# Kernel optimization log

Hardware: AMD Instinct MI355X
Metric: run time of the kernel (lower is better)

Reference implementation:

```python
import jax, jax.numpy as jnp
import numpy as np

B, Q, C, H, N, D, F = 1, 2048, 2048, 1024, 16, 64, 4096
R = Q + C  # relative position encoding length
EPS = 1e-12
NEG = 1e30


def setup_inputs() -> dict:
    key = jax.random.key(0)
    ks = jax.random.split(key, 16)
    s = 0.02
    return dict(
        content_stream=jax.random.normal(ks[0], (B, Q, H), jnp.float32),
        content_mask=jnp.zeros((B, 1, Q, C), jnp.float32),
        context=jax.random.normal(ks[1], (B, C, H), jnp.float32),
        position_encoding=jax.random.normal(ks[2], (B, R, H), jnp.float32),
        content_bias=jax.random.normal(ks[3], (N, D), jnp.float32) * s,
        position_bias=jax.random.normal(ks[4], (N, D), jnp.float32) * s,
        segment_encoding=jax.random.normal(ks[5], (2, N, D), jnp.float32) * s,
        segment_matrix=jax.random.randint(ks[6], (B, Q, C), 0, 2).astype(bool),
        segment_bias=jax.random.normal(ks[7], (N, D), jnp.float32) * s,
        Wq=jax.random.normal(ks[8], (H, N, D), jnp.float32) * s,
        Wk=jax.random.normal(ks[9], (H, N, D), jnp.float32) * s,
        Wv=jax.random.normal(ks[10], (H, N, D), jnp.float32) * s,
        Wr=jax.random.normal(ks[11], (H, N, D), jnp.float32) * s,
        Wo=jax.random.normal(ks[12], (H, N, D), jnp.float32) * s,
        ln1_gamma=jnp.ones((H,), jnp.float32),
        ln1_beta=jnp.zeros((H,), jnp.float32),
        W1=jax.random.normal(ks[13], (H, F), jnp.float32) * s,
        b1=jnp.zeros((F,), jnp.float32),
        W2=jax.random.normal(ks[14], (F, H), jnp.float32) * s,
        b2=jnp.zeros((H,), jnp.float32),
        ln2_gamma=jnp.ones((H,), jnp.float32),
        ln2_beta=jnp.zeros((H,), jnp.float32),
    )


def _layernorm(x, g, b):
    m = jnp.mean(x, axis=-1, keepdims=True)
    v = jnp.mean(jnp.square(x - m), axis=-1, keepdims=True)
    return (x - m) * jax.lax.rsqrt(v + EPS) * g + b


def _rel_shift(x, klen):
    # x: [b, n, q, r] -> shifted [b, n, q, klen] (XLNet reshape trick)
    b, n, q, r = x.shape
    x = x.reshape(b, n, r, q)[:, :, 1:, :].reshape(b, n, q, r - 1)
    return x[:, :, :, :klen]


def reference(content_stream, content_mask, context, position_encoding,
              content_bias, position_bias, segment_encoding, segment_matrix,
              segment_bias, Wq, Wk, Wv, Wr, Wo, ln1_gamma, ln1_beta,
              W1, b1, W2, b2, ln2_gamma, ln2_beta):
    q = jnp.einsum('bqh,hnd->bqnd', content_stream, Wq)
    k = jnp.einsum('bch,hnd->bcnd', context, Wk)
    v = jnp.einsum('bch,hnd->bcnd', context, Wv)
    r = jnp.einsum('brh,hnd->brnd', position_encoding, Wr)

    # content / position / segment bias terms (XLNet relative attention)
    ac = jnp.einsum('bqnd,bcnd->bnqc', q + content_bias, k)
    bd = _rel_shift(jnp.einsum('bqnd,brnd->bnqr', q + position_bias, r),
                    k.shape[1])
    ef = jnp.einsum('bqnd,snd->bnqs', q + segment_bias, segment_encoding)
    ef = jnp.where(segment_matrix[:, None], ef[..., 1:], ef[..., :1])

    scores = (ac + bd + ef) / jnp.sqrt(jnp.float32(D))
    scores = scores - NEG * content_mask  # mask: 1.0 = disallowed
    probs = jax.nn.softmax(scores, axis=-1)

    attn = jnp.einsum('bnqc,bcnd->bqnd', probs, v)
    attn_out = jnp.einsum('bqnd,hnd->bqh', attn, Wo)

    # residual + LN, then FFN, residual + LN (dropout off: training=False)
    ffn_in = _layernorm(attn_out + content_stream, ln1_gamma, ln1_beta)
    ffn_out = jax.nn.relu(ffn_in @ W1 + b1) @ W2 + b2
    return _layernorm(ffn_out + ffn_in, ln2_gamma, ln2_beta)
```

## Files before the change

kernel.cpp:

```cpp
#include <hip/hip_runtime.h>
#include <stdint.h>


typedef unsigned short ushort_t;
typedef __attribute__((ext_vector_type(8))) short bf16x8;
typedef __attribute__((ext_vector_type(4))) float f32x4;

#define QLEN 2048
#define CLEN 2048
#define HDIM 1024
#define NHEAD 16
#define DHEAD 64
#define RLEN 4096
#define FDIM 4096

__device__ __forceinline__ float bf2f(ushort_t u) {
  union { float f; uint32_t i; } x; x.i = ((uint32_t)u) << 16; return x.f;
}
__device__ __forceinline__ ushort_t f2bf(float f) {
  union { float f; uint32_t i; } x; x.f = f;
  uint32_t r = x.i + 0x7fffu + ((x.i >> 16) & 1u);
  return (ushort_t)(r >> 16);
}
__device__ __forceinline__ f32x4 mfma16(bf16x8 a, bf16x8 b, f32x4 c) {
  return __builtin_amdgcn_mfma_f32_16x16x32_bf16(a, b, c, 0, 0, 0);
}
__device__ __forceinline__ bool probe_bf16(const uint32_t* probe) {
  return probe[0] == 0x3F803F80u;
}

typedef const __attribute__((address_space(1))) void* gas_t;
typedef __attribute__((address_space(3))) void* las_t;
__device__ __forceinline__ void glds16(const void* g, void* l) {
  __builtin_amdgcn_global_load_lds((gas_t)(uintptr_t)g, (las_t)(uintptr_t)l, 16, 0, 0);
}

__device__ __forceinline__ void bar_lds() {
  __asm__ volatile("s_waitcnt lgkmcnt(0)\n\ts_barrier" ::: "memory");
}
__device__ __forceinline__ void bar_full() {
  __asm__ volatile("s_waitcnt vmcnt(0) lgkmcnt(0)\n\ts_barrier" ::: "memory");
}

struct ConvJobs {
  const void* src[5];
  const void* mask_src;
  ushort_t* dst[5];
  int n[5];
  int blk0[6];
};

__global__ __launch_bounds__(256) void conv_all(
    ConvJobs J, const uint32_t* __restrict__ probe)
{
  const bool isb = probe_bf16(probe);
  int j = 0;
  #pragma unroll
  for (int t = 1; t < 5; t++) if ((int)blockIdx.x >= J.blk0[t]) j = t;
  const int lb = blockIdx.x - J.blk0[j];
  const int nb = J.blk0[j + 1] - J.blk0[j];
  const int n = J.n[j];
  ushort_t* dst = J.dst[j];
  if (j < 4) {
    const void* src = J.src[j];
    for (int i = lb * 256 + threadIdx.x; i < n; i += nb * 256)
      dst[i] = isb ? ((const ushort_t*)src)[i] : f2bf(((const float*)src)[i]);
  } else {
    const void* sm = J.src[4];
    uint32_t sw = 0;
    #pragma unroll
    for (int t = 0; t < 8; t++) sw |= ((const uint32_t*)sm)[t];
    const bool i8 = sw > 1u;
    for (int i = lb * 256 + threadIdx.x; i < n; i += nb * 256) {
      const int s = i8 ? (int)((const unsigned char*)sm)[i]
                       : (int)((const uint32_t*)sm)[i];
      const float mv = isb ? bf2f(((const ushort_t*)J.mask_src)[i])
                           : ((const float*)J.mask_src)[i];
      const float f = (float)(s ? 1 : 0) + (mv != 0.f ? 2.f : 0.f);
      dst[i] = f2bf(f);
    }
  }
}

struct SmallBatch {
  const void* src[10];
  int n[10];
  int off[10];
};

__global__ __launch_bounds__(256) void convert_small(
    SmallBatch sb, ushort_t* __restrict__ dst, const uint32_t* __restrict__ probe)
{
  const bool isb = probe_bf16(probe);
  const int t = blockIdx.x;
  const void* s = sb.src[t];
  ushort_t* d = dst + sb.off[t];
  for (int i = threadIdx.x; i < sb.n[t]; i += 256)
    d[i] = isb ? ((const ushort_t*)s)[i] : f2bf(((const float*)s)[i]);
}

struct TransJobs { const void* src[4]; ushort_t* dst[4]; };
__global__ __launch_bounds__(256) void transpose4_to_bf16(
    TransJobs T, int R, int C, const uint32_t* __restrict__ probe)
{
  const bool isb = probe_bf16(probe);
  const void* in = T.src[blockIdx.z];
  ushort_t* out = T.dst[blockIdx.z];
  __shared__ ushort_t t[32][33];
  const int bx = blockIdx.x * 32, by = blockIdx.y * 32;
  const int x = threadIdx.x & 31, y0 = threadIdx.x >> 5;
  #pragma unroll
  for (int yy = 0; yy < 32; yy += 8) {
    const size_t idx = (size_t)(by + y0 + yy) * C + bx + x;
    t[y0 + yy][x] = isb ? ((const ushort_t*)in)[idx] : f2bf(((const float*)in)[idx]);
  }
  __syncthreads();
  #pragma unroll
  for (int yy = 0; yy < 32; yy += 8)
    out[(size_t)(bx + y0 + yy) * R + by + x] = t[x][y0 + yy];
}

__global__ __launch_bounds__(256) void transpose_to_bf16(
    const void* __restrict__ in, ushort_t* __restrict__ out, int R, int C,
    const uint32_t* __restrict__ probe)
{
  const bool isb = probe_bf16(probe);
  __shared__ ushort_t t[32][33];
  const int bx = blockIdx.x * 32, by = blockIdx.y * 32;
  const int x = threadIdx.x & 31, y0 = threadIdx.x >> 5;
  #pragma unroll
  for (int yy = 0; yy < 32; yy += 8) {
    const size_t idx = (size_t)(by + y0 + yy) * C + bx + x;
    t[y0 + yy][x] = isb ? ((const ushort_t*)in)[idx] : f2bf(((const float*)in)[idx]);
  }
  __syncthreads();
  #pragma unroll
  for (int yy = 0; yy < 32; yy += 8)
    out[(size_t)(bx + y0 + yy) * R + by + x] = t[x][y0 + yy];
}

__device__ __forceinline__ void gemm_store(
    void* out, const ushort_t* bias, int M, int N, int epi,
    int gm, int gn, float v)
{
  if (epi == 0) {
    ((ushort_t*)out)[(size_t)gm * N + gn] = f2bf(v);
  } else if (epi == 1) {
    ((ushort_t*)out)[(size_t)gn * M + gm] = f2bf(v);
  } else if (epi == 2) {
    ((float*)out)[(size_t)gm * N + gn] = v;
  } else if (epi == 3) {
    v += bf2f(bias[gn]); v = v > 0.f ? v : 0.f;
    ((ushort_t*)out)[(size_t)gm * N + gn] = f2bf(v);
  } else if (epi == 4) {
    v += bf2f(bias[gn]);
    ((float*)out)[(size_t)gm * N + gn] = v;
  } else if (epi == 5) {
    ((ushort_t*)out)[((size_t)(gn >> 6) * M + gm) * 64 + (gn & 63)] = f2bf(v);
  } else {
    if (gn < 1024)
      ((ushort_t*)out)[((size_t)(gn >> 6) * M + gm) * 64 + (gn & 63)] = f2bf(v);
    else
      ((ushort_t*)out)[(size_t)2097152 + (size_t)(gn - 1024) * M + gm] = f2bf(v);
  }
}

__global__ __launch_bounds__(256) void gemm_bt_kernel(
    const ushort_t* __restrict__ A, const ushort_t* __restrict__ Bt,
    const ushort_t* __restrict__ bias, void* __restrict__ out,
    int M, int N, int K, int epi)
{
  __shared__ __attribute__((aligned(16))) ushort_t As[2][128 * 32];
  __shared__ __attribute__((aligned(16))) ushort_t Bs[2][64 * 32];
  const int tid = threadIdx.x;
  const int lane = tid & 63, wave = tid >> 6;
  const int l15 = lane & 15, quad = lane >> 4;
  const int m0 = blockIdx.y * 128, n0 = blockIdx.x * 64;

  const int arow = tid >> 2;
  const int acol = (tid & 3) * 8;

  f32x4 acc[2][4];
  #pragma unroll
  for (int i = 0; i < 2; i++)
    #pragma unroll
    for (int j = 0; j < 4; j++) acc[i][j] = (f32x4){0.f, 0.f, 0.f, 0.f};

  const int KI = K >> 5;
  glds16(&A[(size_t)(m0 + arow) * K + acol], &As[0][tid * 8]);
  glds16(&A[(size_t)(m0 + arow + 64) * K + acol], &As[0][tid * 8 + 2048]);
  glds16(&Bt[(size_t)(n0 + arow) * K + acol], &Bs[0][tid * 8]);
  bar_full();

  for (int ki = 0; ki < KI; ki++) {
    const int b = ki & 1;
    if (ki + 1 < KI) {
      const int k1 = (ki + 1) << 5;
      glds16(&A[(size_t)(m0 + arow) * K + k1 + acol], &As[b ^ 1][tid * 8]);
      glds16(&A[(size_t)(m0 + arow + 64) * K + k1 + acol], &As[b ^ 1][tid * 8 + 2048]);
      glds16(&Bt[(size_t)(n0 + arow) * K + k1 + acol], &Bs[b ^ 1][tid * 8]);
    }
    bf16x8 af[2], bfr[4];
    #pragma unroll
    for (int i = 0; i < 2; i++)
      af[i] = *(const bf16x8*)&As[b][(wave * 32 + i * 16 + l15) * 32 + quad * 8];
    #pragma unroll
    for (int j = 0; j < 4; j++)
      bfr[j] = *(const bf16x8*)&Bs[b][(j * 16 + l15) * 32 + quad * 8];
    #pragma unroll
    for (int i = 0; i < 2; i++)
      #pragma unroll
      for (int j = 0; j < 4; j++)
        acc[i][j] = mfma16(af[i], bfr[j], acc[i][j]);
    bar_full();
  }

  #pragma unroll
  for (int i = 0; i < 2; i++)
    #pragma unroll
    for (int j = 0; j < 4; j++)
      #pragma unroll
      for (int rg = 0; rg < 4; rg++)
        gemm_store(out, bias, M, N, epi,
                   m0 + wave * 32 + i * 16 + quad * 4 + rg,
                   n0 + j * 16 + l15, acc[i][j][rg]);
}

struct Ptr4 { void* p[4]; };
__global__ __launch_bounds__(256) void gemm128_bt_kernel(
    const ushort_t* __restrict__ A, const ushort_t* __restrict__ Bt,
    const ushort_t* __restrict__ bias, Ptr4 outs,
    int M, int N, int K, int Kc, int epi)
{
  __shared__ __attribute__((aligned(16))) ushort_t As[2][128 * 32];
  __shared__ __attribute__((aligned(16))) ushort_t Bs[2][128 * 32];
  const int tid = threadIdx.x;
  const int lane = tid & 63, wave = tid >> 6;
  const int l15 = lane & 15, quad = lane >> 4;
  const int wm = wave >> 1, wn = wave & 1;
  const int m0 = blockIdx.y * 128, n0 = blockIdx.x * 128;
  const int kb = blockIdx.z * Kc;
  void* out = outs.p[blockIdx.z];

  const int arow = tid >> 2;
  const int acol = (tid & 3) * 8;

  f32x4 acc[4][4];
  #pragma unroll
  for (int i = 0; i < 4; i++)
    #pragma unroll
    for (int j = 0; j < 4; j++) acc[i][j] = (f32x4){0.f, 0.f, 0.f, 0.f};

  const int KI = Kc >> 5;
  glds16(&A[(size_t)(m0 + arow) * K + kb + acol], &As[0][tid * 8]);
  glds16(&A[(size_t)(m0 + arow + 64) * K + kb + acol], &As[0][tid * 8 + 2048]);
  glds16(&Bt[(size_t)(n0 + arow) * K + kb + acol], &Bs[0][tid * 8]);
  glds16(&Bt[(size_t)(n0 + arow + 64) * K + kb + acol], &Bs[0][tid * 8 + 2048]);
  bar_full();

  for (int ki = 0; ki < KI; ki++) {
    const int b = ki & 1;
    if (ki + 1 < KI) {
      const int k1 = kb + ((ki + 1) << 5);
      glds16(&A[(size_t)(m0 + arow) * K + k1 + acol], &As[b ^ 1][tid * 8]);
      glds16(&A[(size_t)(m0 + arow + 64) * K + k1 + acol], &As[b ^ 1][tid * 8 + 2048]);
      glds16(&Bt[(size_t)(n0 + arow) * K + k1 + acol], &Bs[b ^ 1][tid * 8]);
      glds16(&Bt[(size_t)(n0 + arow + 64) * K + k1 + acol], &Bs[b ^ 1][tid * 8 + 2048]);
    }
    bf16x8 af[4], bfr[4];
    #pragma unroll
    for (int i = 0; i < 4; i++)
      af[i] = *(const bf16x8*)&As[b][(wm * 64 + i * 16 + l15) * 32 + quad * 8];
    #pragma unroll
    for (int j = 0; j < 4; j++)
      bfr[j] = *(const bf16x8*)&Bs[b][(wn * 64 + j * 16 + l15) * 32 + quad * 8];
    #pragma unroll
    for (int i = 0; i < 4; i++)
      #pragma unroll
      for (int j = 0; j < 4; j++)
        acc[i][j] = mfma16(af[i], bfr[j], acc[i][j]);
    bar_full();
  }

  #pragma unroll
  for (int i = 0; i < 4; i++)
    #pragma unroll
    for (int j = 0; j < 4; j++)
      #pragma unroll
      for (int rg = 0; rg < 4; rg++)
        gemm_store(out, bias, M, N, epi,
                   m0 + wm * 64 + i * 16 + quad * 4 + rg,
                   n0 + wn * 64 + j * 16 + l15, acc[i][j][rg]);
}

__global__ __launch_bounds__(256) void gemm64_bt_kernel(
    const ushort_t* __restrict__ A, const ushort_t* __restrict__ Bt,
    const ushort_t* __restrict__ bias, void* __restrict__ out,
    int M, int N, int K, int epi)
{
  __shared__ __attribute__((aligned(16))) ushort_t As[2][64 * 32];
  __shared__ __attribute__((aligned(16))) ushort_t Bs[2][64 * 32];
  const int tid = threadIdx.x;
  const int lane = tid & 63, wave = tid >> 6;
  const int l15 = lane & 15, quad = lane >> 4;
  const int wm = wave >> 1, wn = wave & 1;
  const int m0 = blockIdx.y * 64, n0 = blockIdx.x * 64;

  const int arow = tid >> 2;
  const int acol = (tid & 3) * 8;

  f32x4 acc[2][2];
  #pragma unroll
  for (int i = 0; i < 2; i++)
    #pragma unroll
    for (int j = 0; j < 2; j++) acc[i][j] = (f32x4){0.f, 0.f, 0.f, 0.f};

  const int KI = K >> 5;
  glds16(&A[(size_t)(m0 + arow) * K + acol], &As[0][tid * 8]);
  glds16(&Bt[(size_t)(n0 + arow) * K + acol], &Bs[0][tid * 8]);
  bar_full();

  for (int ki = 0; ki < KI; ki++) {
    const int b = ki & 1;
    if (ki + 1 < KI) {
      const int k1 = (ki + 1) << 5;
      glds16(&A[(size_t)(m0 + arow) * K + k1 + acol], &As[b ^ 1][tid * 8]);
      glds16(&Bt[(size_t)(n0 + arow) * K + k1 + acol], &Bs[b ^ 1][tid * 8]);
    }
    bf16x8 af[2], bfr[2];
    #pragma unroll
    for (int i = 0; i < 2; i++)
      af[i] = *(const bf16x8*)&As[b][(wm * 32 + i * 16 + l15) * 32 + quad * 8];
    #pragma unroll
    for (int j = 0; j < 2; j++)
      bfr[j] = *(const bf16x8*)&Bs[b][(wn * 32 + j * 16 + l15) * 32 + quad * 8];
    #pragma unroll
    for (int i = 0; i < 2; i++)
      #pragma unroll
      for (int j = 0; j < 2; j++)
        acc[i][j] = mfma16(af[i], bfr[j], acc[i][j]);
    bar_full();
  }

  #pragma unroll
  for (int i = 0; i < 2; i++)
    #pragma unroll
    for (int j = 0; j < 2; j++)
      #pragma unroll
      for (int rg = 0; rg < 4; rg++)
        gemm_store(out, bias, M, N, epi,
                   m0 + wm * 32 + i * 16 + quad * 4 + rg,
                   n0 + wn * 32 + j * 16 + l15, acc[i][j][rg]);
}

#define ESTR 36
#define PSTR2 72
__global__ __launch_bounds__(256, 2) void attn_flash(
    const ushort_t* __restrict__ qh, const ushort_t* __restrict__ kh,
    const ushort_t* __restrict__ vT, const ushort_t* __restrict__ rh,
    const ushort_t* __restrict__ cbias, const ushort_t* __restrict__ pbias,
    const ushort_t* __restrict__ sbias, const ushort_t* __restrict__ senc,
    const ushort_t* __restrict__ fmb, ushort_t* __restrict__ attn)
{
  __shared__ __attribute__((aligned(16))) ushort_t kbuf[2][64 * 64];
  __shared__ __attribute__((aligned(16))) ushort_t vbuf[2][64 * 64];
  __shared__ __attribute__((aligned(16))) ushort_t rbuf[2][96 * 64];
  __shared__ __attribute__((aligned(16))) ushort_t Pbuf[32 * PSTR2];
  __shared__ __attribute__((aligned(16))) float escr[4 * 16 * ESTR];
  __shared__ float wsum[4][32];
  __shared__ float e0s[32], e1s[32];

  const int n = blockIdx.x;
  const int q0 = blockIdx.y * 32;
  const int tid = threadIdx.x;
  const int lane = tid & 63, wave = tid >> 6;
  const int l15 = lane & 15, quad = lane >> 4;

  const ushort_t* qn = qh + (size_t)n * QLEN * 64;
  const ushort_t* kn = kh + (size_t)n * CLEN * 64;
  const ushort_t* rn = rh + (size_t)n * RLEN * 64;
  const ushort_t* vn = vT + (size_t)n * 64 * CLEN;

  const int srow = lane >> 3;
  const int sg = (lane & 7) ^ srow;

  ushort_t* qpcS = (ushort_t*)escr;
  ushort_t* qppS = qpcS + 32 * 64;
  for (int idx = tid; idx < 32 * 64; idx += 256) {
    const int row = idx >> 6, col = idx & 63;
    const float qv = bf2f(qn[(size_t)(q0 + row) * 64 + col]);
    qpcS[idx] = f2bf(qv + bf2f(cbias[n * DHEAD + col]));
    qppS[idx] = f2bf(qv + bf2f(pbias[n * DHEAD + col]));
  }
  if (wave == 3) {
    const int row = lane & 31, sidx = lane >> 5;
    float a = 0.f;
    for (int d = 0; d < DHEAD; d++)
      a += (bf2f(qn[(size_t)(q0 + row) * 64 + d]) + bf2f(sbias[n * DHEAD + d]))
           * bf2f(senc[(size_t)(sidx * NHEAD + n) * DHEAD + d]);
    if (sidx == 0) e0s[row] = a; else e1s[row] = a;
  }
  __syncthreads();

  const bf16x8* qpc8 = (const bf16x8*)qpcS;
  const bf16x8* qpp8 = (const bf16x8*)qppS;
  bf16x8 qcf[2][2], qpf[2][2];
  #pragma unroll
  for (int hq = 0; hq < 2; hq++)
    #pragma unroll
    for (int h = 0; h < 2; h++) {
      qcf[hq][h] = qpc8[(hq * 16 + l15) * 8 + h * 4 + quad];
      qpf[hq][h] = qpp8[(hq * 16 + l15) * 8 + h * 4 + quad];
    }

  {
    const int c0 = 0, ua = c0 - q0 + (QLEN - 32);
    if (wave == 0) {
      #pragma unroll
      for (int i = 0; i < 8; i++)
        glds16(kn + (size_t)(c0 + i * 8 + srow) * 64 + sg * 8, &kbuf[0][i * 512]);
    } else if (wave == 1) {
      #pragma unroll
      for (int i = 0; i < 8; i++)
        glds16(vn + (size_t)(i * 8 + srow) * CLEN + c0 + sg * 8, &vbuf[0][i * 512]);
    } else if (wave == 2) {
      #pragma unroll
      for (int i = 0; i < 8; i++)
        glds16(rn + (size_t)(ua + i * 8 + srow) * 64 + sg * 8, &rbuf[0][i * 512]);
    } else {
      #pragma unroll
      for (int i = 0; i < 4; i++)
        glds16(rn + (size_t)(ua + 64 + i * 8 + srow) * 64 + sg * 8, &rbuf[0][(64 + i * 8) * 64]);
    }
  }
  bar_full();

  float a0q[2], adq[2];
  #pragma unroll
  for (int hq = 0; hq < 2; hq++) {
    const float e0 = e0s[hq * 16 + l15], e1 = e1s[hq * 16 + l15];
    a0q[hq] = e0 * 0.125f;
    adq[hq] = (e1 - e0) * 0.125f;
  }

  float* escr_w = escr + wave * (16 * ESTR);
  const int gk0 = quad ^ (l15 & 7);
  const int gk1 = (quad + 4) ^ (l15 & 7);

  float l_row[2] = {0.f, 0.f};
  f32x4 O[2];
  O[0] = (f32x4){0.f, 0.f, 0.f, 0.f};
  O[1] = (f32x4){0.f, 0.f, 0.f, 0.f};

  const size_t eo0 = (size_t)(q0 + l15) * CLEN + wave * 16 + quad * 4;
  const size_t eo1 = eo0 + (size_t)16 * CLEN;

  for (int ci = 0; ci < CLEN / 64; ci++) {
    const int b = ci & 1;

    uint2 fmv[2];
    fmv[0] = *(const uint2*)&fmb[eo0 + (size_t)ci * 64];
    fmv[1] = *(const uint2*)&fmb[eo1 + (size_t)ci * 64];

    if (ci + 1 < CLEN / 64) {
      const int c1 = (ci + 1) * 64, ua1 = c1 - q0 + (QLEN - 32);
      if (wave == 0) {
        #pragma unroll
        for (int i = 0; i < 8; i++)
          glds16(kn + (size_t)(c1 + i * 8 + srow) * 64 + sg * 8, &kbuf[b ^ 1][i * 512]);
      } else if (wave == 1) {
        #pragma unroll
        for (int i = 0; i < 8; i++)
          glds16(vn + (size_t)(i * 8 + srow) * CLEN + c1 + sg * 8, &vbuf[b ^ 1][i * 512]);
      } else if (wave == 2) {
        #pragma unroll
        for (int i = 0; i < 8; i++)
          glds16(rn + (size_t)(ua1 + i * 8 + srow) * 64 + sg * 8, &rbuf[b ^ 1][i * 512]);
      } else {
        #pragma unroll
        for (int i = 0; i < 4; i++)
          glds16(rn + (size_t)(ua1 + 64 + i * 8 + srow) * 64 + sg * 8, &rbuf[b ^ 1][(64 + i * 8) * 64]);
      }
    }

    const int krow = wave * 16 + l15;
    const bf16x8 kf0 = *(const bf16x8*)&kbuf[b][krow * 64 + gk0 * 8];
    const bf16x8 kf1 = *(const bf16x8*)&kbuf[b][krow * 64 + gk1 * 8];

    #pragma unroll
    for (int hq = 0; hq < 2; hq++) {
      #pragma unroll
      for (int t = 0; t < 2; t++) {
        const int rrow = wave * 16 + ((1 - hq) + t) * 16 + l15;
        f32x4 e = (f32x4){0.f, 0.f, 0.f, 0.f};
        e = mfma16(*(const bf16x8*)&rbuf[b][rrow * 64 + gk0 * 8], qpf[hq][0], e);
        e = mfma16(*(const bf16x8*)&rbuf[b][rrow * 64 + gk1 * 8], qpf[hq][1], e);
        *(f32x4*)&escr_w[l15 * ESTR + t * 16 + quad * 4] = e;
      }

      f32x4 a = (f32x4){0.f, 0.f, 0.f, 0.f};
      a = mfma16(kf0, qcf[hq][0], a);
      a = mfma16(kf1, qcf[hq][1], a);

      const uint2 fv = fmv[hq];
      const ushort_t fm4[4] = {(ushort_t)(fv.x & 0xffff), (ushort_t)(fv.x >> 16),
                               (ushort_t)(fv.y & 0xffff), (ushort_t)(fv.y >> 16)};
      const float* dg = &escr_w[l15 * ESTR + quad * 4 - l15 + 16];
      float p[4], psum = 0.f;
      #pragma unroll
      for (int rg = 0; rg < 4; rg++) {
        const float f = bf2f(fm4[rg]);
        const float mk = floorf(f * 0.5f);
        const float sm = f - 2.f * mk;
        float v = fmaf(a[rg] + dg[rg], 0.125f, fmaf(sm, adq[hq], a0q[hq]));
        v = fmaf(mk, -1.0e30f, v);
        p[rg] = __expf(v);
        psum += p[rg];
      }
      psum += __shfl_xor(psum, 16);
      psum += __shfl_xor(psum, 32);
      l_row[hq] += psum;

      uint2 pk;
      pk.x = (uint32_t)f2bf(p[0]) | ((uint32_t)f2bf(p[1]) << 16);
      pk.y = (uint32_t)f2bf(p[2]) | ((uint32_t)f2bf(p[3]) << 16);
      *(uint2*)&Pbuf[(hq * 16 + l15) * PSTR2 + wave * 16 + quad * 4] = pk;
    }
    bar_lds();

    const int vrow = wave * 16 + l15;
    const bf16x8 vf0 = *(const bf16x8*)&vbuf[b][vrow * 64 + gk0 * 8];
    const bf16x8 vf1 = *(const bf16x8*)&vbuf[b][vrow * 64 + gk1 * 8];
    #pragma unroll
    for (int hq = 0; hq < 2; hq++) {
      const bf16x8 pa0 = *(const bf16x8*)&Pbuf[(hq * 16 + l15) * PSTR2 + quad * 8];
      const bf16x8 pa1 = *(const bf16x8*)&Pbuf[(hq * 16 + l15) * PSTR2 + 32 + quad * 8];
      O[hq] = mfma16(pa0, vf0, O[hq]);
      O[hq] = mfma16(pa1, vf1, O[hq]);
    }

    bar_full();
  }

  if (quad == 0) { wsum[wave][l15] = l_row[0]; wsum[wave][16 + l15] = l_row[1]; }
  __syncthreads();
  #pragma unroll
  for (int hq = 0; hq < 2; hq++) {
    const int qi = hq * 16 + l15;
    const float l = wsum[0][qi] + wsum[1][qi] + wsum[2][qi] + wsum[3][qi];
    const float linv = 1.0f / l;
    float linv4[4];
    #pragma unroll
    for (int rg = 0; rg < 4; rg++) linv4[rg] = __shfl(linv, quad * 4 + rg);
    #pragma unroll
    for (int rg = 0; rg < 4; rg++)
      attn[(size_t)(q0 + hq * 16 + quad * 4 + rg) * HDIM + n * 64 + wave * 16 + l15] =
          f2bf(O[hq][rg] * linv4[rg]);
  }
}

__global__ __launch_bounds__(256) void ln_kernel(
    const float* __restrict__ x0, const float* __restrict__ x1,
    const float* __restrict__ x2, const float* __restrict__ x3,
    const ushort_t* __restrict__ res_bf, const float* __restrict__ res_f,
    const ushort_t* __restrict__ badd,
    const ushort_t* __restrict__ gamma, const ushort_t* __restrict__ beta,
    ushort_t* __restrict__ out_bf, float* __restrict__ out_f,
    void* __restrict__ out_dyn, const uint32_t* __restrict__ probe)
{
  const int row = blockIdx.x, tid = threadIdx.x;
  const int lane = tid & 63, wave = tid >> 6;
  __shared__ float red[8];
  const size_t base = (size_t)row * HDIM;
  float v[4];
  #pragma unroll
  for (int i = 0; i < 4; i++) {
    const int h = tid + i * 256;
    float xv = x0[base + h];
    if (x1) xv += x1[base + h] + x2[base + h] + x3[base + h];
    if (badd) xv += bf2f(badd[h]);
    const float rv = res_bf ? bf2f(res_bf[base + h]) : res_f[base + h];
    v[i] = xv + rv;
  }
  float s = v[0] + v[1] + v[2] + v[3];
  float ss = v[0] * v[0] + v[1] * v[1] + v[2] * v[2] + v[3] * v[3];
  #pragma unroll
  for (int off = 32; off > 0; off >>= 1) {
    s += __shfl_xor(s, off);
    ss += __shfl_xor(ss, off);
  }
  if (lane == 0) { red[wave] = s; red[4 + wave] = ss; }
  __syncthreads();
  s = red[0] + red[1] + red[2] + red[3];
  ss = red[4] + red[5] + red[6] + red[7];
  const float mean = s * (1.0f / HDIM);
  float var = ss * (1.0f / HDIM) - mean * mean;
  var = var > 0.f ? var : 0.f;
  const float rs = rsqrtf(var + 1e-12f);
  const bool outb = out_dyn ? probe_bf16(probe) : false;
  #pragma unroll
  for (int i = 0; i < 4; i++) {
    const int h = tid + i * 256;
    const float y = (v[i] - mean) * rs * bf2f(gamma[h]) + bf2f(beta[h]);
    if (out_bf) out_bf[base + h] = f2bf(y);
    if (out_f)  out_f[base + h] = y;
    if (out_dyn) {
      if (outb) ((ushort_t*)out_dyn)[base + h] = f2bf(y);
      else      ((float*)out_dyn)[base + h] = y;
    }
  }
}

extern "C" void kernel_launch(void* const* d_in, const int* in_sizes, int n_in,
                              void* d_out, int out_size, void* d_ws, size_t ws_size,
                              hipStream_t stream)
{
  (void)in_sizes; (void)n_in; (void)out_size; (void)ws_size;

  const void* cs_r   = d_in[0];
  const void* mask_r = d_in[1];
  const void* ctx_r  = d_in[2];
  const void* pe_r   = d_in[3];
  const void* cb_r   = d_in[4];
  const void* pb_r   = d_in[5];
  const void* senc_r = d_in[6];
  const void* smat   = d_in[7];
  const void* sb_r   = d_in[8];
  const void* Wq_r   = d_in[9];
  const void* Wk_r   = d_in[10];
  const void* Wv_r   = d_in[11];
  const void* Wr_r   = d_in[12];
  const void* Wo_r   = d_in[13];
  const void* g1_r   = d_in[14];
  const void* be1_r  = d_in[15];
  const void* W1_r   = d_in[16];
  const void* b1_r   = d_in[17];
  const void* W2_r   = d_in[18];
  const void* b2_r   = d_in[19];
  const void* g2_r   = d_in[20];
  const void* be2_r  = d_in[21];

  const uint32_t* probe = (const uint32_t*)g1_r;

  char* w = (char*)d_ws;
  #define WSOFF(mb) ((void*)(w + ((size_t)(mb) << 20)))
  ushort_t* fm_b     = (ushort_t*)WSOFF(0);
  ushort_t* Wqt      = (ushort_t*)WSOFF(8);
  ushort_t* Wkt      = (ushort_t*)WSOFF(10);
  ushort_t* Wvt      = (ushort_t*)WSOFF(12);
  ushort_t* Wrt      = (ushort_t*)WSOFF(14);
  ushort_t* W1t      = (ushort_t*)WSOFF(16);
  ushort_t* W2t      = (ushort_t*)WSOFF(24);
  ushort_t* Wo_b     = (ushort_t*)WSOFF(32);
  ushort_t* smalls   = (ushort_t*)WSOFF(34);
  ushort_t* cs_b     = (ushort_t*)WSOFF(35);
  ushort_t* ctx_b    = (ushort_t*)WSOFF(47);
  ushort_t* pe_b     = (ushort_t*)WSOFF(51);
  ushort_t* qbuf     = (ushort_t*)WSOFF(59);
  ushort_t* kbuf     = (ushort_t*)WSOFF(63);
  ushort_t* vTbuf    = (ushort_t*)WSOFF(67);
  ushort_t* rbuf     = (ushort_t*)WSOFF(71);
  ushort_t* attnbuf  = (ushort_t*)WSOFF(79);
  float*    attn_out = (float*)WSOFF(83);
  ushort_t* ffn_in_b = (ushort_t*)WSOFF(91);
  ushort_t* hidden   = (ushort_t*)WSOFF(39);
  float*    ffn_in_f = (float*)WSOFF(71);
  float*    fp0      = (float*)WSOFF(0);
  float*    fp1      = (float*)WSOFF(8);
  float*    fp2      = (float*)WSOFF(59);
  float*    fp3      = (float*)WSOFF(83);

  ushort_t* cb   = smalls + 0;
  ushort_t* pb   = smalls + 1024;
  ushort_t* sb   = smalls + 2048;
  ushort_t* senc = smalls + 3072;
  ushort_t* b1   = smalls + 5120;
  ushort_t* b2   = smalls + 9216;
  ushort_t* g1   = smalls + 10240;
  ushort_t* be1  = smalls + 11264;
  ushort_t* g2   = smalls + 12288;
  ushort_t* be2  = smalls + 13312;

  const dim3 blk(256);

  SmallBatch sbatch;
  const void* ssrc[10] = {cb_r, pb_r, sb_r, senc_r, b1_r, b2_r, g1_r, be1_r, g2_r, be2_r};
  const int   sn[10]   = {1024, 1024, 1024, 2048, 4096, 1024, 1024, 1024, 1024, 1024};
  const int   soff[10] = {0, 1024, 2048, 3072, 5120, 9216, 10240, 11264, 12288, 13312};
  for (int i = 0; i < 10; i++) { sbatch.src[i] = ssrc[i]; sbatch.n[i] = sn[i]; sbatch.off[i] = soff[i]; }
  convert_small<<<10, blk, 0, stream>>>(sbatch, smalls, probe);

  ConvJobs cj;
  cj.src[0] = cs_r;  cj.dst[0] = cs_b;  cj.n[0] = QLEN * HDIM;
  cj.src[1] = ctx_r; cj.dst[1] = ctx_b; cj.n[1] = CLEN * HDIM;
  cj.src[2] = pe_r;  cj.dst[2] = pe_b;  cj.n[2] = RLEN * HDIM;
  cj.src[3] = Wo_r;  cj.dst[3] = Wo_b;  cj.n[3] = HDIM * HDIM;
  cj.src[4] = smat;  cj.dst[4] = fm_b;  cj.n[4] = QLEN * CLEN;
  cj.mask_src = mask_r;
  int pfx = 0;
  for (int i = 0; i < 5; i++) {
    cj.blk0[i] = pfx;
    pfx += (cj.n[i] + 2047) / 2048;
  }
  cj.blk0[5] = pfx;
  conv_all<<<pfx, blk, 0, stream>>>(cj, probe);

  TransJobs tj;
  tj.src[0] = Wq_r; tj.dst[0] = Wqt;
  tj.src[1] = Wk_r; tj.dst[1] = Wkt;
  tj.src[2] = Wv_r; tj.dst[2] = Wvt;
  tj.src[3] = Wr_r; tj.dst[3] = Wrt;
  transpose4_to_bf16<<<dim3(32, 32, 4), blk, 0, stream>>>(tj, HDIM, HDIM, probe);
  transpose_to_bf16<<<dim3(128, 32), blk, 0, stream>>>(W1_r, W1t, HDIM, FDIM, probe);
  transpose_to_bf16<<<dim3(32, 128), blk, 0, stream>>>(W2_r, W2t, FDIM, HDIM, probe);

  gemm64_bt_kernel<<<dim3(16, 32), blk, 0, stream>>>(cs_b,  Wqt, nullptr, qbuf,  QLEN, HDIM, HDIM, 5);
  gemm_bt_kernel<<<dim3(32, 16), blk, 0, stream>>>(ctx_b, Wkt, nullptr, kbuf, CLEN, 2048, HDIM, 6);
  gemm_bt_kernel<<<dim3(16, 32), blk, 0, stream>>>(pe_b,  Wrt, nullptr, rbuf,  RLEN, HDIM, HDIM, 5);

  attn_flash<<<dim3(NHEAD, QLEN / 32), blk, 0, stream>>>(
      qbuf, kbuf, vTbuf, rbuf, cb, pb, sb, senc, fm_b, attnbuf);

  gemm64_bt_kernel<<<dim3(16, 32), blk, 0, stream>>>(attnbuf, Wo_b, nullptr, attn_out, QLEN, HDIM, HDIM, 2);

  ln_kernel<<<QLEN, blk, 0, stream>>>(attn_out, nullptr, nullptr, nullptr,
                                      cs_b, nullptr, nullptr, g1, be1,
                                      ffn_in_b, ffn_in_f, nullptr, probe);

  Ptr4 o1; o1.p[0] = hidden; o1.p[1] = o1.p[2] = o1.p[3] = nullptr;
  gemm128_bt_kernel<<<dim3(32, 16, 1), blk, 0, stream>>>(
      ffn_in_b, W1t, b1, o1, QLEN, FDIM, HDIM, HDIM, 3);

  Ptr4 o2; o2.p[0] = fp0; o2.p[1] = fp1; o2.p[2] = fp2; o2.p[3] = fp3;
  gemm128_bt_kernel<<<dim3(8, 16, 4), blk, 0, stream>>>(
      hidden, W2t, nullptr, o2, QLEN, HDIM, FDIM, FDIM / 4, 2);

  ln_kernel<<<QLEN, blk, 0, stream>>>(fp0, fp1, fp2, fp3,
                                      nullptr, ffn_in_f, b2, g2, be2,
                                      nullptr, nullptr, d_out, probe);
  #undef WSOFF
}
```

Baseline: 489.8 us.

## Split attention query halves across eight waves per block

The attention kernel now launches 512 threads per block instead of 256. The 2x2 query-half loop is spread over eight waves, so each wave handles one 16-row query half and one 16-column key slice, and the K/V/R tile loads are split across all eight waves. This roughly halves the per-wave serial work and register pressure and raises the number of waves that can hide latency. In exchange it adds shared scratch, doubles the waves taking part in each barrier, and issues smaller load chunks per wave.

Result: faster. 475.4 us (-2.9%).

```diff
diff --git a/kernel.cpp b/kernel.cpp
--- a/kernel.cpp
+++ b/kernel.cpp
@@ -355,7 +355,7 @@
 
 #define ESTR 36
 #define PSTR2 72
-__global__ __launch_bounds__(256, 2) void attn_flash(
+__global__ __launch_bounds__(512, 4) void attn_flash(
     const ushort_t* __restrict__ qh, const ushort_t* __restrict__ kh,
     const ushort_t* __restrict__ vT, const ushort_t* __restrict__ rh,
     const ushort_t* __restrict__ cbias, const ushort_t* __restrict__ pbias,
@@ -366,8 +366,8 @@
   __shared__ __attribute__((aligned(16))) ushort_t vbuf[2][64 * 64];
   __shared__ __attribute__((aligned(16))) ushort_t rbuf[2][96 * 64];
   __shared__ __attribute__((aligned(16))) ushort_t Pbuf[32 * PSTR2];
-  __shared__ __attribute__((aligned(16))) float escr[4 * 16 * ESTR];
-  __shared__ float wsum[4][32];
+  __shared__ __attribute__((aligned(16))) float escr[8 * 16 * ESTR];
+  __shared__ float wsum[2][4][16];
   __shared__ float e0s[32], e1s[32];
 
   const int n = blockIdx.x;
@@ -375,6 +375,7 @@
   const int tid = threadIdx.x;
   const int lane = tid & 63, wave = tid >> 6;
   const int l15 = lane & 15, quad = lane >> 4;
+  const int hq = wave >> 2, ct = wave & 3;
 
   const ushort_t* qn = qh + (size_t)n * QLEN * 64;
   const ushort_t* kn = kh + (size_t)n * CLEN * 64;
@@ -386,13 +387,13 @@
 
   ushort_t* qpcS = (ushort_t*)escr;
   ushort_t* qppS = qpcS + 32 * 64;
-  for (int idx = tid; idx < 32 * 64; idx += 256) {
+  for (int idx = tid; idx < 32 * 64; idx += 512) {
     const int row = idx >> 6, col = idx & 63;
     const float qv = bf2f(qn[(size_t)(q0 + row) * 64 + col]);
     qpcS[idx] = f2bf(qv + bf2f(cbias[n * DHEAD + col]));
     qppS[idx] = f2bf(qv + bf2f(pbias[n * DHEAD + col]));
   }
-  if (wave == 3) {
+  if (wave == 7) {
     const int row = lane & 31, sidx = lane >> 5;
     float a = 0.f;
     for (int d = 0; d < DHEAD; d++)
@@ -404,159 +405,134 @@
 
   const bf16x8* qpc8 = (const bf16x8*)qpcS;
   const bf16x8* qpp8 = (const bf16x8*)qppS;
-  bf16x8 qcf[2][2], qpf[2][2];
-  #pragma unroll
-  for (int hq = 0; hq < 2; hq++)
-    #pragma unroll
-    for (int h = 0; h < 2; h++) {
-      qcf[hq][h] = qpc8[(hq * 16 + l15) * 8 + h * 4 + quad];
-      qpf[hq][h] = qpp8[(hq * 16 + l15) * 8 + h * 4 + quad];
-    }
+  bf16x8 qcf[2], qpf[2];
+  #pragma unroll
+  for (int h = 0; h < 2; h++) {
+    qcf[h] = qpc8[(hq * 16 + l15) * 8 + h * 4 + quad];
+    qpf[h] = qpp8[(hq * 16 + l15) * 8 + h * 4 + quad];
+  }
 
   {
     const int c0 = 0, ua = c0 - q0 + (QLEN - 32);
-    if (wave == 0) {
-      #pragma unroll
-      for (int i = 0; i < 8; i++)
-        glds16(kn + (size_t)(c0 + i * 8 + srow) * 64 + sg * 8, &kbuf[0][i * 512]);
-    } else if (wave == 1) {
-      #pragma unroll
-      for (int i = 0; i < 8; i++)
-        glds16(vn + (size_t)(i * 8 + srow) * CLEN + c0 + sg * 8, &vbuf[0][i * 512]);
-    } else if (wave == 2) {
-      #pragma unroll
-      for (int i = 0; i < 8; i++)
-        glds16(rn + (size_t)(ua + i * 8 + srow) * 64 + sg * 8, &rbuf[0][i * 512]);
+    if (wave < 2) {
+      const int r0 = wave * 32;
+      #pragma unroll
+      for (int i = 0; i < 4; i++)
+        glds16(kn + (size_t)(c0 + r0 + i * 8 + srow) * 64 + sg * 8, &kbuf[0][(r0 + i * 8) * 64]);
+    } else if (wave < 4) {
+      const int r0 = (wave - 2) * 32;
+      #pragma unroll
+      for (int i = 0; i < 4; i++)
+        glds16(vn + (size_t)(r0 + i * 8 + srow) * CLEN + c0 + sg * 8, &vbuf[0][(r0 + i * 8) * 64]);
     } else {
-      #pragma unroll
-      for (int i = 0; i < 4; i++)
-        glds16(rn + (size_t)(ua + 64 + i * 8 + srow) * 64 + sg * 8, &rbuf[0][(64 + i * 8) * 64]);
+      const int r0 = (wave - 4) * 24;
+      #pragma unroll
+      for (int i = 0; i < 3; i++)
+        glds16(rn + (size_t)(ua + r0 + i * 8 + srow) * 64 + sg * 8, &rbuf[0][(r0 + i * 8) * 64]);
     }
   }
   bar_full();
 
-  float a0q[2], adq[2];
-  #pragma unroll
-  for (int hq = 0; hq < 2; hq++) {
-    const float e0 = e0s[hq * 16 + l15], e1 = e1s[hq * 16 + l15];
-    a0q[hq] = e0 * 0.125f;
-    adq[hq] = (e1 - e0) * 0.125f;
-  }
+  const float e0v = e0s[hq * 16 + l15], e1v = e1s[hq * 16 + l15];
+  const float a0q = e0v * 0.125f;
+  const float adq = (e1v - e0v) * 0.125f;
 
   float* escr_w = escr + wave * (16 * ESTR);
   const int gk0 = quad ^ (l15 & 7);
   const int gk1 = (quad + 4) ^ (l15 & 7);
 
-  float l_row[2] = {0.f, 0.f};
-  f32x4 O[2];
-  O[0] = (f32x4){0.f, 0.f, 0.f, 0.f};
-  O[1] = (f32x4){0.f, 0.f, 0.f, 0.f};
-
-  const size_t eo0 = (size_t)(q0 + l15) * CLEN + wave * 16 + quad * 4;
-  const size_t eo1 = eo0 + (size_t)16 * CLEN;
+  float l_row = 0.f;
+  f32x4 O = (f32x4){0.f, 0.f, 0.f, 0.f};
+
+  const size_t eoff = (size_t)(q0 + hq * 16 + l15) * CLEN + ct * 16 + quad * 4;
 
   for (int ci = 0; ci < CLEN / 64; ci++) {
     const int b = ci & 1;
 
-    uint2 fmv[2];
-    fmv[0] = *(const uint2*)&fmb[eo0 + (size_t)ci * 64];
-    fmv[1] = *(const uint2*)&fmb[eo1 + (size_t)ci * 64];
+    const uint2 fmv = *(const uint2*)&fmb[eoff + (size_t)ci * 64];
 
     if (ci + 1 < CLEN / 64) {
       const int c1 = (ci + 1) * 64, ua1 = c1 - q0 + (QLEN - 32);
-      if (wave == 0) {
-        #pragma unroll
-        for (int i = 0; i < 8; i++)
-          glds16(kn + (size_t)(c1 + i * 8 + srow) * 64 + sg * 8, &kbuf[b ^ 1][i * 512]);
-      } else if (wave == 1) {
-        #pragma unroll
-        for (int i = 0; i < 8; i++)
-          glds16(vn + (size_t)(i * 8 + srow) * CLEN + c1 + sg * 8, &vbuf[b ^ 1][i * 512]);
-      } else if (wave == 2) {
-        #pragma unroll
-        for (int i = 0; i < 8; i++)
-          glds16(rn + (size_t)(ua1 + i * 8 + srow) * 64 + sg * 8, &rbuf[b ^ 1][i * 512]);
-      } else {
+      if (wave < 2) {
+        const int r0 = wave * 32;
         #pragma unroll
         for (int i = 0; i < 4; i++)
-          glds16(rn + (size_t)(ua1 + 64 + i * 8 + srow) * 64 + sg * 8, &rbuf[b ^ 1][(64 + i * 8) * 64]);
+          glds16(kn + (size_t)(c1 + r0 + i * 8 + srow) * 64 + sg * 8, &kbuf[b ^ 1][(r0 + i * 8) * 64]);
+      } else if (wave < 4) {
+        const int r0 = (wave - 2) * 32;
+        #pragma unroll
+        for (int i = 0; i < 4; i++)
+          glds16(vn + (size_t)(r0 + i * 8 + srow) * CLEN + c1 + sg * 8, &vbuf[b ^ 1][(r0 + i * 8) * 64]);
+      } else {
+        const int r0 = (wave - 4) * 24;
+        #pragma unroll
+        for (int i = 0; i < 3; i++)
+          glds16(rn + (size_t)(ua1 + r0 + i * 8 + srow) * 64 + sg * 8, &rbuf[b ^ 1][(r0 + i * 8) * 64]);
       }
     }
 
-    const int krow = wave * 16 + l15;
-    const bf16x8 kf0 = *(const bf16x8*)&kbuf[b][krow * 64 + gk0 * 8];
-    const bf16x8 kf1 = *(const bf16x8*)&kbuf[b][krow * 64 + gk1 * 8];
-
-    #pragma unroll
-    for (int hq = 0; hq < 2; hq++) {
-      #pragma unroll
-      for (int t = 0; t < 2; t++) {
-        const int rrow = wave * 16 + ((1 - hq) + t) * 16 + l15;
-        f32x4 e = (f32x4){0.f, 0.f, 0.f, 0.f};
-        e = mfma16(*(const bf16x8*)&rbuf[b][rrow * 64 + gk0 * 8], qpf[hq][0], e);
-        e = mfma16(*(const bf16x8*)&rbuf[b][rrow * 64 + gk1 * 8], qpf[hq][1], e);
-        *(f32x4*)&escr_w[l15 * ESTR + t * 16 + quad * 4] = e;
-      }
-
-      f32x4 a = (f32x4){0.f, 0.f, 0.f, 0.f};
-      a = mfma16(kf0, qcf[hq][0], a);
-      a = mfma16(kf1, qcf[hq][1], a);
-
-      const uint2 fv = fmv[hq];
-      const ushort_t fm4[4] = {(ushort_t)(fv.x & 0xffff), (ushort_t)(fv.x >> 16),
-                               (ushort_t)(fv.y & 0xffff), (ushort_t)(fv.y >> 16)};
-      const float* dg = &escr_w[l15 * ESTR + quad * 4 - l15 + 16];
-      float p[4], psum = 0.f;
-      #pragma unroll
-      for (int rg = 0; rg < 4; rg++) {
-        const float f = bf2f(fm4[rg]);
-        const float mk = floorf(f * 0.5f);
-        const float sm = f - 2.f * mk;
-        float v = fmaf(a[rg] + dg[rg], 0.125f, fmaf(sm, adq[hq], a0q[hq]));
-        v = fmaf(mk, -1.0e30f, v);
-        p[rg] = __expf(v);
-        psum += p[rg];
-      }
-      psum += __shfl_xor(psum, 16);
-      psum += __shfl_xor(psum, 32);
-      l_row[hq] += psum;
-
+    #pragma unroll
+    for (int t = 0; t < 2; t++) {
+      const int rrow = ct * 16 + ((1 - hq) + t) * 16 + l15;
+      f32x4 e = (f32x4){0.f, 0.f, 0.f, 0.f};
+      e = mfma16(*(const bf16x8*)&rbuf[b][rrow * 64 + gk0 * 8], qpf[0], e);
+      e = mfma16(*(const bf16x8*)&rbuf[b][rrow * 64 + gk1 * 8], qpf[1], e);
+      *(f32x4*)&escr_w[l15 * ESTR + t * 16 + quad * 4] = e;
+    }
+
+    const int krow = ct * 16 + l15;
+    f32x4 a = (f32x4){0.f, 0.f, 0.f, 0.f};
+    a = mfma16(*(const bf16x8*)&kbuf[b][krow * 64 + gk0 * 8], qcf[0], a);
+    a = mfma16(*(const bf16x8*)&kbuf[b][krow * 64 + gk1 * 8], qcf[1], a);
+
+    const ushort_t fm4[4] = {(ushort_t)(fmv.x & 0xffff), (ushort_t)(fmv.x >> 16),
+                             (ushort_t)(fmv.y & 0xffff), (ushort_t)(fmv.y >> 16)};
+    const float* dg = &escr_w[l15 * ESTR + quad * 4 - l15 + 16];
+    float p[4], psum = 0.f;
+    #pragma unroll
+    for (int rg = 0; rg < 4; rg++) {
+      const float f = bf2f(fm4[rg]);
+      const float mk = floorf(f * 0.5f);
+      const float sm = f - 2.f * mk;
+      float v = fmaf(a[rg] + dg[rg], 0.125f, fmaf(sm, adq, a0q));
+      v = fmaf(mk, -1.0e30f, v);
+      p[rg] = __expf(v);
+      psum += p[rg];
+    }
+    psum += __shfl_xor(psum, 16);
+    psum += __shfl_xor(psum, 32);
+    l_row += psum;
+
+    {
       uint2 pk;
       pk.x = (uint32_t)f2bf(p[0]) | ((uint32_t)f2bf(p[1]) << 16);
       pk.y = (uint32_t)f2bf(p[2]) | ((uint32_t)f2bf(p[3]) << 16);
-      *(uint2*)&Pbuf[(hq * 16 + l15) * PSTR2 + wave * 16 + quad * 4] = pk;
+      *(uint2*)&Pbuf[(hq * 16 + l15) * PSTR2 + ct * 16 + quad * 4] = pk;
     }
     bar_lds();
 
-    const int vrow = wave * 16 + l15;
+    const int vrow = ct * 16 + l15;
     const bf16x8 vf0 = *(const bf16x8*)&vbuf[b][vrow * 64 + gk0 * 8];
     const bf16x8 vf1 = *(const bf16x8*)&vbuf[b][vrow * 64 + gk1 * 8];
-    #pragma unroll
-    for (int hq = 0; hq < 2; hq++) {
-      const bf16x8 pa0 = *(const bf16x8*)&Pbuf[(hq * 16 + l15) * PSTR2 + quad * 8];
-      const bf16x8 pa1 = *(const bf16x8*)&Pbuf[(hq * 16 + l15) * PSTR2 + 32 + quad * 8];
-      O[hq] = mfma16(pa0, vf0, O[hq]);
-      O[hq] = mfma16(pa1, vf1, O[hq]);
-    }
+    const bf16x8 pa0 = *(const bf16x8*)&Pbuf[(hq * 16 + l15) * PSTR2 + quad * 8];
+    const bf16x8 pa1 = *(const bf16x8*)&Pbuf[(hq * 16 + l15) * PSTR2 + 32 + quad * 8];
+    O = mfma16(pa0, vf0, O);
+    O = mfma16(pa1, vf1, O);
 
     bar_full();
   }
 
-  if (quad == 0) { wsum[wave][l15] = l_row[0]; wsum[wave][16 + l15] = l_row[1]; }
+  if (quad == 0) wsum[hq][ct][l15] = l_row;
   __syncthreads();
-  #pragma unroll
-  for (int hq = 0; hq < 2; hq++) {
-    const int qi = hq * 16 + l15;
-    const float l = wsum[0][qi] + wsum[1][qi] + wsum[2][qi] + wsum[3][qi];
-    const float linv = 1.0f / l;
-    float linv4[4];
-    #pragma unroll
-    for (int rg = 0; rg < 4; rg++) linv4[rg] = __shfl(linv, quad * 4 + rg);
-    #pragma unroll
-    for (int rg = 0; rg < 4; rg++)
-      attn[(size_t)(q0 + hq * 16 + quad * 4 + rg) * HDIM + n * 64 + wave * 16 + l15] =
-          f2bf(O[hq][rg] * linv4[rg]);
-  }
+  const float l = wsum[hq][0][l15] + wsum[hq][1][l15] + wsum[hq][2][l15] + wsum[hq][3][l15];
+  const float linv = 1.0f / l;
+  float linv4[4];
+  #pragma unroll
+  for (int rg = 0; rg < 4; rg++) linv4[rg] = __shfl(linv, quad * 4 + rg);
+  #pragma unroll
+  for (int rg = 0; rg < 4; rg++)
+    attn[(size_t)(q0 + hq * 16 + quad * 4 + rg) * HDIM + n * 64 + ct * 16 + l15] =
+        f2bf(O[rg] * linv4[rg]);
 }
 
 __global__ __launch_bounds__(256) void ln_kernel(
@@ -718,7 +694,7 @@
   gemm_bt_kernel<<<dim3(32, 16), blk, 0, stream>>>(ctx_b, Wkt, nullptr, kbuf, CLEN, 2048, HDIM, 6);
   gemm_bt_kernel<<<dim3(16, 32), blk, 0, stream>>>(pe_b,  Wrt, nullptr, rbuf,  RLEN, HDIM, HDIM, 5);
 
-  attn_flash<<<dim3(NHEAD, QLEN / 32), blk, 0, stream>>>(
+  attn_flash<<<dim3(NHEAD, QLEN / 32), dim3(512), 0, stream>>>(
       qbuf, kbuf, vTbuf, rbuf, cb, pb, sb, senc, fm_b, attnbuf);
 
   gemm64_bt_kernel<<<dim3(16, 32), blk, 0, stream>>>(attnbuf, Wo_b, nullptr, attn_out, QLEN, HDIM, HDIM, 2);
```
